# Optimization experiments

Measured on AMD Instinct MI355X. Metric: run time of the kernel, lower is better.

Reference implementation:

```python
import jax, jax.numpy as jnp
import numpy as np

V, H, D, L, B = 512, 8, 64, 16, 4096
F1, F2, F3 = 64, 64, 8
EPS = 1e-6


def setup_inputs() -> dict:
    ks = jax.random.split(jax.random.key(0), 8)
    inputs = jax.random.randint(ks[0], (B, L), 0, V, dtype=jnp.int32)
    emb = jax.random.normal(ks[1], (V, D), jnp.float32) * 0.02
    w_qkv = jax.random.normal(ks[2], (D, 3 * H * D), jnp.float32) * (1.0 / np.sqrt(D))
    ln_gamma = jnp.ones((D,), jnp.float32)
    ln_beta = jnp.zeros((D,), jnp.float32)
    w1 = jax.random.normal(ks[3], (H, F1), jnp.float32) * (1.0 / np.sqrt(H))
    b1 = jnp.zeros((F1,), jnp.float32)
    w2 = jax.random.normal(ks[4], (F1, F2), jnp.float32) * (1.0 / np.sqrt(F1))
    b2 = jnp.zeros((F2,), jnp.float32)
    w3 = jax.random.normal(ks[5], (F2, F3), jnp.float32) * (1.0 / np.sqrt(F2))
    b3 = jnp.zeros((F3,), jnp.float32)
    return dict(inputs=inputs, emb=emb, w_qkv=w_qkv, ln_gamma=ln_gamma,
                ln_beta=ln_beta, w1=w1, b1=b1, w2=w2, b2=b2, w3=w3, b3=b3,
                n_words=8, n_names=128)


def _layernorm(x, g, b):
    mu = x.mean(-1, keepdims=True)
    var = ((x - mu) ** 2).mean(-1, keepdims=True)
    return (x - mu) / jnp.sqrt(var + EPS) * g + b


def reference(inputs, emb, w_qkv, ln_gamma, ln_beta, w1, b1, w2, b2, w3, b3,
              n_words, n_names):
    # padding_idx=0: zero row 0 of the embedding table
    emb0 = emb.at[0].set(0.0)
    # char-level q,k,v: [V, H, D] each
    qkv = (emb0 @ w_qkv).reshape(V, 3 * H, D)
    q, k, v = qkv[:, :H], qkv[:, H:2 * H], qkv[:, 2 * H:]
    # per-head char similarity table [H, V, V]
    sim = jnp.einsum('qhd,khd->hqk', q, k) / np.sqrt(D).astype(np.float32)
    sim = sim.at[:, :, 0].set(-1e9)  # mask attending TO pad char
    # gather per-word similarities: [H, B, L, L] -> [B, H, L, L]
    inputs_sim = sim[:, inputs[:, :, None], inputs[:, None, :]]
    inputs_sim = jnp.transpose(inputs_sim, (1, 0, 2, 3))
    attn = jax.nn.softmax(inputs_sim, axis=-1)  # dropout is eval-mode identity
    vv = v[inputs]  # [B, L, H, D]
    out = jnp.einsum('bhij,bjhd->bihd', attn, vv)  # [B, L, H, D]
    out = _layernorm(out, ln_gamma, ln_beta)
    # MLP over the head axis: [B, L, D, H] -> [B, L, D, F3]
    x = jnp.swapaxes(out, 2, 3)
    x = jax.nn.relu(x @ w1 + b1)
    x = jax.nn.relu(x @ w2 + b2)
    x = x @ w3 + b3
    char_ft = x.reshape(B, L, D * F3)
    # masked mean over chars -> word features [B, D*F3]
    mask = (inputs != 0).astype(jnp.float32)
    word_ft = jnp.einsum('bl,blf->bf', mask, char_ft) / mask.sum(-1, keepdims=True)
    # mean over words of each name, then group names
    name_ft = word_ft.reshape(B // n_words, n_words, -1).mean(1)
    return name_ft.reshape(-1, n_names, name_ft.shape[-1])
```

## Files before the change

### kernel.cpp

```cpp
#include <hip/hip_runtime.h>
#include <hip/hip_bf16.h>
#include <stdint.h>

#define V 512
#define H 8
#define D 64
#define L 16
#define B 4096

typedef __attribute__((ext_vector_type(8))) short short8;
typedef __attribute__((ext_vector_type(4))) float float4_t;

union __attribute__((aligned(16))) Frag { uint32_t u[4]; short8 s; };

__device__ __forceinline__ void split_hl(float x, uint32_t& hi, uint32_t& lo) {
    uint32_t uu = __float_as_uint(x);
    hi = uu >> 16;
    float fl = x - __uint_as_float(uu & 0xffff0000u);
    lo = __float_as_uint(fl) >> 16;
}
__device__ __forceinline__ uint32_t pack_hl(float x) {
    uint32_t uu = __float_as_uint(x);
    uint32_t ha = uu & 0xffff0000u;
    float fl = x - __uint_as_float(ha);
    return ha | (__float_as_uint(fl) >> 16);
}
__device__ __forceinline__ uint32_t pack_lh(float x) {
    uint32_t uu = __float_as_uint(x);
    uint32_t ha = uu & 0xffff0000u;
    float fl = x - __uint_as_float(ha);
    return (uu >> 16) | (__float_as_uint(fl) & 0xffff0000u);
}

__global__ __launch_bounds__(256) void qkv_kernel(const float* __restrict__ emb,
                                                  const float* __restrict__ w_qkv,
                                                  float* __restrict__ qkv)
{
    const int c = blockIdx.x * 256 + threadIdx.x;
    const int vbase = blockIdx.y * 64;
    float wcol[64];
#pragma unroll
    for (int k = 0; k < 64; ++k) wcol[k] = w_qkv[k * 1536 + c];
    for (int v = vbase; v < vbase + 64; ++v) {
        if (v == 0) { qkv[c] = 0.0f; continue; }
        float acc = 0.0f;
#pragma unroll
        for (int k = 0; k < 64; ++k) acc = fmaf(emb[v * 64 + k], wcol[k], acc);
        qkv[v * 1536 + c] = acc;
    }
}

__global__ __launch_bounds__(256) void sim_kernel(const float* __restrict__ qkv,
                                                  float* __restrict__ sim)
{
    const int t = threadIdx.x;
    const int qb = blockIdx.x, kb = blockIdx.y, h = blockIdx.z;
    const int kj = t & 63;
    const int r0 = __builtin_amdgcn_readfirstlane(t >> 6);

    const float* kbase = qkv + (kb * 64 + kj) * 1536 + 512 + h * 64;
    float kv[64];
#pragma unroll
    for (int m = 0; m < 16; ++m)
        *(float4*)&kv[m * 4] = *(const float4*)&kbase[m * 4];

    const float* qbase = qkv + (qb * 64 + r0 * 16) * 1536 + h * 64;
    float acc[16];
#pragma unroll
    for (int ii = 0; ii < 16; ++ii) acc[ii] = 0.0f;
#pragma unroll
    for (int ii = 0; ii < 16; ++ii) {
#pragma unroll
        for (int m = 0; m < 16; ++m) {
            float4 q4 = *(const float4*)&qbase[ii * 1536 + m * 4];
            acc[ii] = fmaf(q4.x, kv[m * 4 + 0], acc[ii]);
            acc[ii] = fmaf(q4.y, kv[m * 4 + 1], acc[ii]);
            acc[ii] = fmaf(q4.z, kv[m * 4 + 2], acc[ii]);
            acc[ii] = fmaf(q4.w, kv[m * 4 + 3], acc[ii]);
        }
    }
    const int kglob = kb * 64 + kj;
#pragma unroll
    for (int ii = 0; ii < 16; ++ii) {
        float val = acc[ii] * 0.125f;
        if (kglob == 0) val = -1.0e9f;
        sim[((qb * 64 + r0 * 16 + ii) * 8 + h) * 512 + kglob] = val;
    }
}

__global__ void prep_kernel(const float* __restrict__ w1,
                            const float* __restrict__ w2,
                            const float* __restrict__ w3,
                            uint32_t* __restrict__ wfrag)
{
    const int lane = threadIdx.x;
    const int lq = lane >> 4, ln = lane & 15;
    uint32_t out[96];
#pragma unroll
    for (int mt = 0; mt < 4; ++mt) {
        const int fout = mt * 16 + ln;
#pragma unroll
        for (int j = 0; j < 4; ++j) {
            uint32_t h0, l0, h1_, l1_;
            split_hl(w1[(2 * j) * 64 + fout], h0, l0);
            split_hl(w1[(2 * j + 1) * 64 + fout], h1_, l1_);
            uint32_t hw = h0 | (h1_ << 16);
            uint32_t lw = l0 | (l1_ << 16);
            out[mt * 4 + j] = (lq == 3) ? 0u : ((lq == 1) ? lw : hw);
        }
    }
#pragma unroll
    for (int mt = 0; mt < 4; ++mt)
#pragma unroll
        for (int s = 0; s < 2; ++s)
#pragma unroll
            for (int j = 0; j < 4; ++j) {
                const int fout = mt * 16 + ln;
                const int fin0 = s * 32 + lq * 8 + 2 * j;
                uint32_t h0, l0, h1_, l1_;
                split_hl(w2[fin0 * 64 + fout], h0, l0);
                split_hl(w2[(fin0 + 1) * 64 + fout], h1_, l1_);
                out[16 + mt * 16 + s * 4 + j]     = h0 | (h1_ << 16);
                out[16 + mt * 16 + 8 + s * 4 + j] = l0 | (l1_ << 16);
            }
#pragma unroll
    for (int s = 0; s < 2; ++s)
#pragma unroll
        for (int j = 0; j < 4; ++j) {
            const int fin0 = s * 32 + lq * 8 + 2 * j;
            float v0 = (ln < 8) ? w3[fin0 * 8 + ln] : 0.0f;
            float v1 = (ln < 8) ? w3[(fin0 + 1) * 8 + ln] : 0.0f;
            uint32_t h0, l0, h1_, l1_;
            split_hl(v0, h0, l0);
            split_hl(v1, h1_, l1_);
            out[80 + s * 4 + j] = h0 | (h1_ << 16);
            out[88 + s * 4 + j] = l0 | (l1_ << 16);
        }
#pragma unroll
    for (int i = 0; i < 96; ++i) wfrag[lane * 96 + i] = out[i];
}

__global__ __launch_bounds__(256, 2) void main_kernel(
    const int* __restrict__ inputs,
    const float* __restrict__ qkv, const float* __restrict__ sim,
    const uint32_t* __restrict__ wfrag,
    const float* __restrict__ gamma, const float* __restrict__ beta,
    const float* __restrict__ b1, const float* __restrict__ b2,
    const float* __restrict__ b3,
    float* __restrict__ wft)
{
    __shared__ int tokS[16];
    __shared__ __align__(16) uint32_t arena[6848];
    __shared__ __align__(16) uint32_t xSu[8192];

    const int t = threadIdx.x;
    const int b = blockIdx.x;
    const int lane = t & 63;
    const int w = t >> 6;
    const int lq = lane >> 4;
    const int ln = lane & 15;
    float* vS = (float*)(arena + 2688);

    if (t < 16) tokS[t] = inputs[b * 16 + t];
    __syncthreads();

    int cnt = 0;
#pragma unroll
    for (int j2 = 0; j2 < 16; ++j2) cnt += (tokS[j2] != 0) ? 1 : 0;
    const float inv_msum = 1.0f / (float)cnt;

    float gam4[4], bet4[4];
#pragma unroll
    for (int dch = 0; dch < 4; ++dch) {
        gam4[dch] = gamma[dch * 16 + ln];
        bet4[dch] = beta[dch * 16 + ln];
    }

    float sg[16];
    if (t < 128) {
        const int i0 = t & 15, h0 = t >> 4;
        const int simrow = (tokS[i0] * 8 + h0) * 512;
#pragma unroll
        for (int j = 0; j < 16; ++j) sg[j] = sim[simrow + tokS[j]];
    }
#pragma unroll
    for (int e4 = 0; e4 < 4; ++e4) {
        int o = e4 * 256 + t;
        int j = o >> 6, hs = (o >> 4) & 3, d4 = o & 15;
        *(float4*)&vS[j * 260 + hs * 64 + d4 * 4] =
            *(const float4*)&qkv[tokS[j] * 1536 + 1024 + hs * 64 + d4 * 4];
    }
    if (t < 128) {
        float m = -3.0e38f;
#pragma unroll
        for (int j = 0; j < 16; ++j) m = fmaxf(m, sg[j]);
        float sum = 0.0f;
#pragma unroll
        for (int j = 0; j < 16; ++j) { sg[j] = __expf(sg[j] - m); sum += sg[j]; }
        float inv = 1.0f / sum;
#pragma unroll
        for (int j = 0; j < 16; ++j) arena[t * 21 + j] = pack_lh(sg[j] * inv);
    }
    __syncthreads();

    const float4_t zf = {0.0f, 0.0f, 0.0f, 0.0f};
    for (int s = 0; s < 2; ++s) {
        if (s == 1) {
            __syncthreads();
#pragma unroll
            for (int e4 = 0; e4 < 4; ++e4) {
                int o = e4 * 256 + t;
                int j = o >> 6, hs = (o >> 4) & 3, d4 = o & 15;
                *(float4*)&vS[j * 260 + hs * 64 + d4 * 4] =
                    *(const float4*)&qkv[tokS[j] * 1536 + 1024 + (4 + hs) * 64 + d4 * 4];
            }
            __syncthreads();
        }
        const int h = 4 * s + w;
        Frag A;
#pragma unroll
        for (int jj = 0; jj < 4; ++jj)
            A.u[jj] = arena[(h * 16 + ln) * 21 + lq * 4 + jj];
        float4_t acc[4];
#pragma unroll
        for (int dch = 0; dch < 4; ++dch) {
            Frag B1, B2;
#pragma unroll
            for (int jj = 0; jj < 4; ++jj) {
                float vv = vS[(lq * 4 + jj) * 260 + w * 64 + dch * 16 + ln];
                uint32_t uu = __float_as_uint(vv);
                B1.u[jj] = (uu >> 16) | (uu & 0xffff0000u);
                float vl = vv - __uint_as_float(uu & 0xffff0000u);
                B2.u[jj] = __float_as_uint(vl) >> 16;
            }
            float4_t a = __builtin_amdgcn_mfma_f32_16x16x32_bf16(A.s, B1.s, zf, 0, 0, 0);
            acc[dch]  = __builtin_amdgcn_mfma_f32_16x16x32_bf16(A.s, B2.s, a, 0, 0, 0);
        }
#pragma unroll
        for (int r = 0; r < 4; ++r) {
            float s1 = acc[0][r] + acc[1][r] + acc[2][r] + acc[3][r];
#pragma unroll
            for (int off = 8; off > 0; off >>= 1) s1 += __shfl_xor(s1, off);
            float mu = s1 * (1.0f / 64.0f);
            float d0 = acc[0][r] - mu, d1 = acc[1][r] - mu;
            float d2 = acc[2][r] - mu, d3 = acc[3][r] - mu;
            float v1 = d0 * d0 + d1 * d1 + d2 * d2 + d3 * d3;
#pragma unroll
            for (int off = 8; off > 0; off >>= 1) v1 += __shfl_xor(v1, off);
            float rinv = 1.0f / sqrtf(v1 * (1.0f / 64.0f) + 1e-6f);
            const int i = lq * 4 + r;
            float dd[4] = {d0, d1, d2, d3};
#pragma unroll
            for (int dch = 0; dch < 4; ++dch) {
                float y = dd[dch] * rinv * gam4[dch] + bet4[dch];
                xSu[i * 512 + h * 64 + ((dch ^ lq) & 3) * 16 + ln] = pack_hl(y);
            }
        }
    }
    __syncthreads();

    uint32_t* h1buf = arena + w * 1088;
    const uint4* wfl4 = (const uint4*)(wfrag + lane * 96);

    Frag A1[4], A2h[4][2], A2l[4][2], A3h[2], A3l[2];
#pragma unroll
    for (int mt = 0; mt < 4; ++mt) *(uint4*)A1[mt].u = wfl4[mt];
#pragma unroll
    for (int mt = 0; mt < 4; ++mt)
#pragma unroll
        for (int s2 = 0; s2 < 2; ++s2) {
            *(uint4*)A2h[mt][s2].u = wfl4[4 + mt * 4 + s2];
            *(uint4*)A2l[mt][s2].u = wfl4[4 + mt * 4 + 2 + s2];
        }
#pragma unroll
    for (int s2 = 0; s2 < 2; ++s2) {
        *(uint4*)A3h[s2].u = wfl4[20 + s2];
        *(uint4*)A3l[s2].u = wfl4[22 + s2];
    }
    float b1v[4][4], b2v[4][4], b3v[4];
#pragma unroll
    for (int mt = 0; mt < 4; ++mt) {
        float4 v1 = ((const float4*)b1)[mt * 4 + lq];
        b1v[mt][0] = v1.x; b1v[mt][1] = v1.y; b1v[mt][2] = v1.z; b1v[mt][3] = v1.w;
        float4 v2 = ((const float4*)b2)[mt * 4 + lq];
        b2v[mt][0] = v2.x; b2v[mt][1] = v2.y; b2v[mt][2] = v2.z; b2v[mt][3] = v2.w;
    }
    {
        float4 v3 = ((const float4*)b3)[lq & 1];
        b3v[0] = v3.x; b3v[1] = v3.y; b3v[2] = v3.z; b3v[3] = v3.w;
    }

    float wacc[4][4];
#pragma unroll
    for (int dc = 0; dc < 4; ++dc)
#pragma unroll
        for (int r = 0; r < 4; ++r) wacc[dc][r] = 0.0f;

#pragma unroll 1
    for (int n6 = 0; n6 < 4; ++n6) {
        const int i = w * 4 + n6;
        if (tokS[i] == 0) continue;
#pragma unroll
        for (int dc = 0; dc < 4; ++dc) {
            uint32_t r8[8];
            const int xb = i * 512 + ((dc ^ (i >> 2)) & 3) * 16 + ln;
#pragma unroll
            for (int h = 0; h < 8; ++h) r8[h] = xSu[xb + h * 64];
            Frag B1;
#pragma unroll
            for (int j = 0; j < 4; ++j) {
                uint32_t hd = (r8[2 * j] >> 16) | (r8[2 * j + 1] & 0xffff0000u);
                uint32_t ld = (r8[2 * j] & 0xffffu) | (r8[2 * j + 1] << 16);
                B1.u[j] = (lq == 3) ? 0u : ((lq == 2) ? ld : hd);
            }
            float4_t acc[4];
#pragma unroll
            for (int mt = 0; mt < 4; ++mt)
                acc[mt] = __builtin_amdgcn_mfma_f32_16x16x32_bf16(A1[mt].s, B1.s, zf, 0, 0, 0);
#pragma unroll
            for (int mt = 0; mt < 4; ++mt) {
                Frag pk;
#pragma unroll
                for (int r = 0; r < 4; ++r)
                    pk.u[r] = pack_hl(fmaxf(acc[mt][r] + b1v[mt][r], 0.0f));
                *(uint4*)&h1buf[ln * 68 + mt * 16 + lq * 4] = *(uint4*)pk.u;
            }
            Frag B2h[2], B2l[2];
#pragma unroll
            for (int s2 = 0; s2 < 2; ++s2) {
                uint4 t0 = *(const uint4*)&h1buf[ln * 68 + s2 * 32 + lq * 8];
                uint4 t1 = *(const uint4*)&h1buf[ln * 68 + s2 * 32 + lq * 8 + 4];
                uint32_t q8[8] = {t0.x, t0.y, t0.z, t0.w, t1.x, t1.y, t1.z, t1.w};
#pragma unroll
                for (int j = 0; j < 4; ++j) {
                    B2h[s2].u[j] = (q8[2 * j] >> 16) | (q8[2 * j + 1] & 0xffff0000u);
                    B2l[s2].u[j] = (q8[2 * j] & 0xffffu) | (q8[2 * j + 1] << 16);
                }
            }
#pragma unroll
            for (int mt = 0; mt < 4; ++mt) {
                float4_t a = zf;
                a = __builtin_amdgcn_mfma_f32_16x16x32_bf16(A2h[mt][0].s, B2h[0].s, a, 0, 0, 0);
                a = __builtin_amdgcn_mfma_f32_16x16x32_bf16(A2l[mt][0].s, B2h[0].s, a, 0, 0, 0);
                a = __builtin_amdgcn_mfma_f32_16x16x32_bf16(A2h[mt][0].s, B2l[0].s, a, 0, 0, 0);
                a = __builtin_amdgcn_mfma_f32_16x16x32_bf16(A2h[mt][1].s, B2h[1].s, a, 0, 0, 0);
                a = __builtin_amdgcn_mfma_f32_16x16x32_bf16(A2l[mt][1].s, B2h[1].s, a, 0, 0, 0);
                a = __builtin_amdgcn_mfma_f32_16x16x32_bf16(A2h[mt][1].s, B2l[1].s, a, 0, 0, 0);
                acc[mt] = a;
            }
#pragma unroll
            for (int mt = 0; mt < 4; ++mt) {
                Frag pk;
#pragma unroll
                for (int r = 0; r < 4; ++r)
                    pk.u[r] = pack_hl(fmaxf(acc[mt][r] + b2v[mt][r], 0.0f));
                *(uint4*)&h1buf[ln * 68 + mt * 16 + lq * 4] = *(uint4*)pk.u;
            }
            float4_t a3 = zf;
#pragma unroll
            for (int s2 = 0; s2 < 2; ++s2) {
                uint4 t0 = *(const uint4*)&h1buf[ln * 68 + s2 * 32 + lq * 8];
                uint4 t1 = *(const uint4*)&h1buf[ln * 68 + s2 * 32 + lq * 8 + 4];
                uint32_t q8[8] = {t0.x, t0.y, t0.z, t0.w, t1.x, t1.y, t1.z, t1.w};
                Frag Bh, Bl;
#pragma unroll
                for (int j = 0; j < 4; ++j) {
                    Bh.u[j] = (q8[2 * j] >> 16) | (q8[2 * j + 1] & 0xffff0000u);
                    Bl.u[j] = (q8[2 * j] & 0xffffu) | (q8[2 * j + 1] << 16);
                }
                a3 = __builtin_amdgcn_mfma_f32_16x16x32_bf16(A3h[s2].s, Bh.s, a3, 0, 0, 0);
                a3 = __builtin_amdgcn_mfma_f32_16x16x32_bf16(A3l[s2].s, Bh.s, a3, 0, 0, 0);
                a3 = __builtin_amdgcn_mfma_f32_16x16x32_bf16(A3h[s2].s, Bl.s, a3, 0, 0, 0);
            }
#pragma unroll
            for (int r = 0; r < 4; ++r) wacc[dc][r] += a3[r] + b3v[r];
        }
    }

    __syncthreads();
    float* partF = (float*)xSu;
    if (lq < 2) {
#pragma unroll
        for (int dc = 0; dc < 4; ++dc)
#pragma unroll
            for (int r = 0; r < 4; ++r)
                partF[w * 512 + (lq * 4 + r) * 64 + dc * 16 + ln] = wacc[dc][r];
    }
    __syncthreads();
#pragma unroll
    for (int rep = 0; rep < 2; ++rep) {
        int f = rep * 256 + t;
        int dd = f >> 3, c = f & 7;
        float s4 = 0.0f;
#pragma unroll
        for (int ww = 0; ww < 4; ++ww) s4 += partF[ww * 512 + c * 64 + dd];
        wft[b * 512 + f] = s4 * inv_msum;
    }
}

__global__ __launch_bounds__(256) void reduce_kernel(const float* __restrict__ wft,
                                                     float* __restrict__ out)
{
    const int o = blockIdx.x * 256 + threadIdx.x;
    const int g = o >> 9, f = o & 511;
    float s = 0.0f;
#pragma unroll
    for (int ww = 0; ww < 8; ++ww) s += wft[(g * 8 + ww) * 512 + f];
    out[o] = s * 0.125f;
}

extern "C" void kernel_launch(void* const* d_in, const int* in_sizes, int n_in,
                              void* d_out, int out_size, void* d_ws, size_t ws_size,
                              hipStream_t stream)
{
    const int*   inputs = (const int*)  d_in[0];
    const float* emb    = (const float*)d_in[1];
    const float* w_qkv  = (const float*)d_in[2];
    const float* gam    = (const float*)d_in[3];
    const float* bet    = (const float*)d_in[4];
    const float* w1     = (const float*)d_in[5];
    const float* b1     = (const float*)d_in[6];
    const float* w2     = (const float*)d_in[7];
    const float* b2     = (const float*)d_in[8];
    const float* w3     = (const float*)d_in[9];
    const float* b3     = (const float*)d_in[10];

    float* qkv = (float*)d_ws;
    float* sim = qkv + 512 * 1536;
    float* wft = sim + 512 * 8 * 512;
    uint32_t* wfrag = (uint32_t*)(wft + 4096 * 512);
    float* out = (float*)d_out;

    qkv_kernel  <<<dim3(6, 8),    256, 0, stream>>>(emb, w_qkv, qkv);
    sim_kernel  <<<dim3(8, 8, 8), 256, 0, stream>>>(qkv, sim);
    prep_kernel <<<1,              64, 0, stream>>>(w1, w2, w3, wfrag);
    main_kernel <<<4096,          256, 0, stream>>>(inputs, qkv, sim, wfrag,
                                                    gam, bet, b1, b2, b3, wft);
    reduce_kernel<<<1024,         256, 0, stream>>>(wft, out);
}
```

Before: 376.2 us.

## Store sim head-innermost and keep MLP activations as separate bf16 hi/lo planes

The similarity table is now written with the head index innermost, so each (i,j) token pair gathers all 8 heads with two float4 loads. Those values are transposed through shared memory for the softmax. The LayerNorm output and the MLP hidden activations are stored as separate bf16 high and low planes in LDS, laid out so MFMA B fragments load directly with uint4 reads instead of being repacked by shuffling bits. The cost is strided scalar writes in sim_kernel, an extra barrier, and more LDS per block.

```diff
diff --git a/kernel.cpp b/kernel.cpp
--- a/kernel.cpp
+++ b/kernel.cpp
@@ -19,18 +19,15 @@
     float fl = x - __uint_as_float(uu & 0xffff0000u);
     lo = __float_as_uint(fl) >> 16;
 }
-__device__ __forceinline__ uint32_t pack_hl(float x) {
-    uint32_t uu = __float_as_uint(x);
-    uint32_t ha = uu & 0xffff0000u;
-    float fl = x - __uint_as_float(ha);
-    return ha | (__float_as_uint(fl) >> 16);
-}
 __device__ __forceinline__ uint32_t pack_lh(float x) {
     uint32_t uu = __float_as_uint(x);
     uint32_t ha = uu & 0xffff0000u;
     float fl = x - __uint_as_float(ha);
     return (uu >> 16) | (__float_as_uint(fl) & 0xffff0000u);
 }
+__device__ __forceinline__ uint32_t pk2(float a, float b) {
+    return (__float_as_uint(a) >> 16) | (__float_as_uint(b) & 0xffff0000u);
+}
 
 __global__ __launch_bounds__(256) void qkv_kernel(const float* __restrict__ emb,
                                                   const float* __restrict__ w_qkv,
@@ -51,7 +48,7 @@
 }
 
 __global__ __launch_bounds__(256) void sim_kernel(const float* __restrict__ qkv,
-                                                  float* __restrict__ sim)
+                                                  float* __restrict__ sim2)
 {
     const int t = threadIdx.x;
     const int qb = blockIdx.x, kb = blockIdx.y, h = blockIdx.z;
@@ -84,7 +81,7 @@
     for (int ii = 0; ii < 16; ++ii) {
         float val = acc[ii] * 0.125f;
         if (kglob == 0) val = -1.0e9f;
-        sim[((qb * 64 + r0 * 16 + ii) * 8 + h) * 512 + kglob] = val;
+        sim2[(size_t)((qb * 64 + r0 * 16 + ii) * 512 + kglob) * 8 + h] = val;
     }
 }
 
@@ -142,7 +139,7 @@
 
 __global__ __launch_bounds__(256, 2) void main_kernel(
     const int* __restrict__ inputs,
-    const float* __restrict__ qkv, const float* __restrict__ sim,
+    const float* __restrict__ qkv, const float* __restrict__ sim2,
     const uint32_t* __restrict__ wfrag,
     const float* __restrict__ gamma, const float* __restrict__ beta,
     const float* __restrict__ b1, const float* __restrict__ b2,
@@ -151,7 +148,7 @@
 {
     __shared__ int tokS[16];
     __shared__ __align__(16) uint32_t arena[6848];
-    __shared__ __align__(16) uint32_t xSu[8192];
+    __shared__ __align__(16) uint32_t planes[8708];
 
     const int t = threadIdx.x;
     const int b = blockIdx.x;
@@ -160,8 +157,10 @@
     const int lq = lane >> 4;
     const int ln = lane & 15;
     float* vS = (float*)(arena + 2688);
+    ushort* up = (ushort*)planes;
 
     if (t < 16) tokS[t] = inputs[b * 16 + t];
+    if (t < 4) planes[4352 + t] = 0u;
     __syncthreads();
 
     int cnt = 0;
@@ -176,30 +175,45 @@
         bet4[dch] = beta[dch * 16 + ln];
     }
 
-    float sg[16];
+    {
+        const int i1 = t >> 4, j1 = t & 15;
+        const float* srow = sim2 + (size_t)(tokS[i1] * 512 + tokS[j1]) * 8;
+        float4 sa = *(const float4*)srow;
+        float4 sb = *(const float4*)(srow + 4);
+#pragma unroll
+        for (int e4 = 0; e4 < 4; ++e4) {
+            int o = e4 * 256 + t;
+            int j = o >> 6, hs = (o >> 4) & 3, d4 = o & 15;
+            *(float4*)&vS[j * 260 + hs * 64 + d4 * 4] =
+                *(const float4*)&qkv[tokS[j] * 1536 + 1024 + hs * 64 + d4 * 4];
+        }
+        float* pS = (float*)planes;
+        pS[(i1 * 8 + 0) * 17 + j1] = sa.x;
+        pS[(i1 * 8 + 1) * 17 + j1] = sa.y;
+        pS[(i1 * 8 + 2) * 17 + j1] = sa.z;
+        pS[(i1 * 8 + 3) * 17 + j1] = sa.w;
+        pS[(i1 * 8 + 4) * 17 + j1] = sb.x;
+        pS[(i1 * 8 + 5) * 17 + j1] = sb.y;
+        pS[(i1 * 8 + 6) * 17 + j1] = sb.z;
+        pS[(i1 * 8 + 7) * 17 + j1] = sb.w;
+    }
+    __syncthreads();
+
     if (t < 128) {
-        const int i0 = t & 15, h0 = t >> 4;
-        const int simrow = (tokS[i0] * 8 + h0) * 512;
-#pragma unroll
-        for (int j = 0; j < 16; ++j) sg[j] = sim[simrow + tokS[j]];
-    }
-#pragma unroll
-    for (int e4 = 0; e4 < 4; ++e4) {
-        int o = e4 * 256 + t;
-        int j = o >> 6, hs = (o >> 4) & 3, d4 = o & 15;
-        *(float4*)&vS[j * 260 + hs * 64 + d4 * 4] =
-            *(const float4*)&qkv[tokS[j] * 1536 + 1024 + hs * 64 + d4 * 4];
-    }
-    if (t < 128) {
+        const float* pS = (const float*)planes;
+        float s[16];
+#pragma unroll
+        for (int j = 0; j < 16; ++j) s[j] = pS[t * 17 + j];
         float m = -3.0e38f;
 #pragma unroll
-        for (int j = 0; j < 16; ++j) m = fmaxf(m, sg[j]);
+        for (int j = 0; j < 16; ++j) m = fmaxf(m, s[j]);
         float sum = 0.0f;
 #pragma unroll
-        for (int j = 0; j < 16; ++j) { sg[j] = __expf(sg[j] - m); sum += sg[j]; }
+        for (int j = 0; j < 16; ++j) { s[j] = __expf(s[j] - m); sum += s[j]; }
         float inv = 1.0f / sum;
-#pragma unroll
-        for (int j = 0; j < 16; ++j) arena[t * 21 + j] = pack_lh(sg[j] * inv);
+        const int prow = (t & 7) * 16 + (t >> 3);
+#pragma unroll
+        for (int j = 0; j < 16; ++j) arena[prow * 21 + j] = pack_lh(s[j] * inv);
     }
     __syncthreads();
 
@@ -253,13 +267,17 @@
 #pragma unroll
             for (int dch = 0; dch < 4; ++dch) {
                 float y = dd[dch] * rinv * gam4[dch] + bet4[dch];
-                xSu[i * 512 + h * 64 + ((dch ^ lq) & 3) * 16 + ln] = pack_hl(y);
-            }
-        }
-    }
-    __syncthreads();
-
-    uint32_t* h1buf = arena + w * 1088;
+                uint32_t uu = __float_as_uint(y);
+                float lo = y - __uint_as_float(uu & 0xffff0000u);
+                const int xi = (dch * 16 + ln) * 136 + i * 8 + h;
+                up[xi] = (ushort)(uu >> 16);
+                up[8712 + xi] = (ushort)(__float_as_uint(lo) >> 16);
+            }
+        }
+    }
+    __syncthreads();
+
+    uint32_t* hb = arena + w * 1152;
     const uint4* wfl4 = (const uint4*)(wfrag + lane * 96);
 
     Frag A1[4], A2h[4][2], A2l[4][2], A3h[2], A3l[2];
@@ -302,40 +320,39 @@
         if (tokS[i] == 0) continue;
 #pragma unroll
         for (int dc = 0; dc < 4; ++dc) {
-            uint32_t r8[8];
-            const int xb = i * 512 + ((dc ^ (i >> 2)) & 3) * 16 + ln;
-#pragma unroll
-            for (int h = 0; h < 8; ++h) r8[h] = xSu[xb + h * 64];
-            Frag B1;
-#pragma unroll
-            for (int j = 0; j < 4; ++j) {
-                uint32_t hd = (r8[2 * j] >> 16) | (r8[2 * j + 1] & 0xffff0000u);
-                uint32_t ld = (r8[2 * j] & 0xffffu) | (r8[2 * j + 1] << 16);
-                B1.u[j] = (lq == 3) ? 0u : ((lq == 2) ? ld : hd);
-            }
+            const int xoff = (dc * 16 + ln) * 68 + i * 4;
+            const int a1 = (lq < 2) ? xoff : ((lq == 2) ? xoff + 4356 : 4352);
+            const uint4 xv = *(const uint4*)&planes[a1];
+            Frag B1; B1.u[0] = xv.x; B1.u[1] = xv.y; B1.u[2] = xv.z; B1.u[3] = xv.w;
+
             float4_t acc[4];
 #pragma unroll
             for (int mt = 0; mt < 4; ++mt)
                 acc[mt] = __builtin_amdgcn_mfma_f32_16x16x32_bf16(A1[mt].s, B1.s, zf, 0, 0, 0);
 #pragma unroll
             for (int mt = 0; mt < 4; ++mt) {
-                Frag pk;
-#pragma unroll
-                for (int r = 0; r < 4; ++r)
-                    pk.u[r] = pack_hl(fmaxf(acc[mt][r] + b1v[mt][r], 0.0f));
-                *(uint4*)&h1buf[ln * 68 + mt * 16 + lq * 4] = *(uint4*)pk.u;
+                float v0 = fmaxf(acc[mt][0] + b1v[mt][0], 0.0f);
+                float v1f = fmaxf(acc[mt][1] + b1v[mt][1], 0.0f);
+                float v2 = fmaxf(acc[mt][2] + b1v[mt][2], 0.0f);
+                float v3f = fmaxf(acc[mt][3] + b1v[mt][3], 0.0f);
+                uint32_t ph0 = pk2(v0, v1f), ph1 = pk2(v2, v3f);
+                float e0 = __uint_as_float(ph0 << 16);
+                float e1 = __uint_as_float(ph0 & 0xffff0000u);
+                float e2 = __uint_as_float(ph1 << 16);
+                float e3 = __uint_as_float(ph1 & 0xffff0000u);
+                uint32_t pl0 = pk2(v0 - e0, v1f - e1), pl1 = pk2(v2 - e2, v3f - e3);
+                const int wa = ln * 36 + mt * 8 + lq * 2;
+                *(uint2*)&hb[wa] = make_uint2(ph0, ph1);
+                *(uint2*)&hb[576 + wa] = make_uint2(pl0, pl1);
             }
             Frag B2h[2], B2l[2];
 #pragma unroll
             for (int s2 = 0; s2 < 2; ++s2) {
-                uint4 t0 = *(const uint4*)&h1buf[ln * 68 + s2 * 32 + lq * 8];
-                uint4 t1 = *(const uint4*)&h1buf[ln * 68 + s2 * 32 + lq * 8 + 4];
-                uint32_t q8[8] = {t0.x, t0.y, t0.z, t0.w, t1.x, t1.y, t1.z, t1.w};
-#pragma unroll
-                for (int j = 0; j < 4; ++j) {
-                    B2h[s2].u[j] = (q8[2 * j] >> 16) | (q8[2 * j + 1] & 0xffff0000u);
-                    B2l[s2].u[j] = (q8[2 * j] & 0xffffu) | (q8[2 * j + 1] << 16);
-                }
+                const int ra = ln * 36 + s2 * 16 + lq * 4;
+                uint4 th = *(const uint4*)&hb[ra];
+                uint4 tl = *(const uint4*)&hb[576 + ra];
+                B2h[s2].u[0] = th.x; B2h[s2].u[1] = th.y; B2h[s2].u[2] = th.z; B2h[s2].u[3] = th.w;
+                B2l[s2].u[0] = tl.x; B2l[s2].u[1] = tl.y; B2l[s2].u[2] = tl.z; B2l[s2].u[3] = tl.w;
             }
 #pragma unroll
             for (int mt = 0; mt < 4; ++mt) {
@@ -350,24 +367,29 @@
             }
 #pragma unroll
             for (int mt = 0; mt < 4; ++mt) {
-                Frag pk;
-#pragma unroll
-                for (int r = 0; r < 4; ++r)
-                    pk.u[r] = pack_hl(fmaxf(acc[mt][r] + b2v[mt][r], 0.0f));
-                *(uint4*)&h1buf[ln * 68 + mt * 16 + lq * 4] = *(uint4*)pk.u;
+                float v0 = fmaxf(acc[mt][0] + b2v[mt][0], 0.0f);
+                float v1f = fmaxf(acc[mt][1] + b2v[mt][1], 0.0f);
+                float v2 = fmaxf(acc[mt][2] + b2v[mt][2], 0.0f);
+                float v3f = fmaxf(acc[mt][3] + b2v[mt][3], 0.0f);
+                uint32_t ph0 = pk2(v0, v1f), ph1 = pk2(v2, v3f);
+                float e0 = __uint_as_float(ph0 << 16);
+                float e1 = __uint_as_float(ph0 & 0xffff0000u);
+                float e2 = __uint_as_float(ph1 << 16);
+                float e3 = __uint_as_float(ph1 & 0xffff0000u);
+                uint32_t pl0 = pk2(v0 - e0, v1f - e1), pl1 = pk2(v2 - e2, v3f - e3);
+                const int wa = ln * 36 + mt * 8 + lq * 2;
+                *(uint2*)&hb[wa] = make_uint2(ph0, ph1);
+                *(uint2*)&hb[576 + wa] = make_uint2(pl0, pl1);
             }
             float4_t a3 = zf;
 #pragma unroll
             for (int s2 = 0; s2 < 2; ++s2) {
-                uint4 t0 = *(const uint4*)&h1buf[ln * 68 + s2 * 32 + lq * 8];
-                uint4 t1 = *(const uint4*)&h1buf[ln * 68 + s2 * 32 + lq * 8 + 4];
-                uint32_t q8[8] = {t0.x, t0.y, t0.z, t0.w, t1.x, t1.y, t1.z, t1.w};
+                const int ra = ln * 36 + s2 * 16 + lq * 4;
+                uint4 th = *(const uint4*)&hb[ra];
+                uint4 tl = *(const uint4*)&hb[576 + ra];
                 Frag Bh, Bl;
-#pragma unroll
-                for (int j = 0; j < 4; ++j) {
-                    Bh.u[j] = (q8[2 * j] >> 16) | (q8[2 * j + 1] & 0xffff0000u);
-                    Bl.u[j] = (q8[2 * j] & 0xffffu) | (q8[2 * j + 1] << 16);
-                }
+                Bh.u[0] = th.x; Bh.u[1] = th.y; Bh.u[2] = th.z; Bh.u[3] = th.w;
+                Bl.u[0] = tl.x; Bl.u[1] = tl.y; Bl.u[2] = tl.z; Bl.u[3] = tl.w;
                 a3 = __builtin_amdgcn_mfma_f32_16x16x32_bf16(A3h[s2].s, Bh.s, a3, 0, 0, 0);
                 a3 = __builtin_amdgcn_mfma_f32_16x16x32_bf16(A3l[s2].s, Bh.s, a3, 0, 0, 0);
                 a3 = __builtin_amdgcn_mfma_f32_16x16x32_bf16(A3h[s2].s, Bl.s, a3, 0, 0, 0);
@@ -378,7 +400,7 @@
     }
 
     __syncthreads();
-    float* partF = (float*)xSu;
+    float* partF = (float*)planes;
     if (lq < 2) {
 #pragma unroll
         for (int dc = 0; dc < 4; ++dc)
@@ -426,15 +448,15 @@
     const float* b3     = (const float*)d_in[10];
 
     float* qkv = (float*)d_ws;
-    float* sim = qkv + 512 * 1536;
-    float* wft = sim + 512 * 8 * 512;
+    float* sim2 = qkv + 512 * 1536;
+    float* wft = sim2 + 512 * 512 * 8;
     uint32_t* wfrag = (uint32_t*)(wft + 4096 * 512);
     float* out = (float*)d_out;
 
     qkv_kernel  <<<dim3(6, 8),    256, 0, stream>>>(emb, w_qkv, qkv);
-    sim_kernel  <<<dim3(8, 8, 8), 256, 0, stream>>>(qkv, sim);
+    sim_kernel  <<<dim3(8, 8, 8), 256, 0, stream>>>(qkv, sim2);
     prep_kernel <<<1,              64, 0, stream>>>(w1, w2, w3, wfrag);
-    main_kernel <<<4096,          256, 0, stream>>>(inputs, qkv, sim, wfrag,
+    main_kernel <<<4096,          256, 0, stream>>>(inputs, qkv, sim2, wfrag,
                                                     gam, bet, b1, b2, b3, wft);
     reduce_kernel<<<1024,         256, 0, stream>>>(wft, out);
 }
```

Result: faster. 337.0 us (-10.4%).
